# Performance work log

Hardware: AMD Instinct MI355X
Metric: run time of the kernel (lower is better)

## Reference

```python
import jax, jax.numpy as jnp
import numpy as np

DF, DK, DG, NR = 1024, 64, 64, 16
DV = DF // NR  # 64
N = 1024       # num_rois


def setup_inputs() -> dict:
    key = jax.random.key(0)
    ks = jax.random.split(key, 12)
    def xavier(k, out_d, in_d):
        lim = float(np.sqrt(6.0 / (in_d + out_d)))
        return jax.random.uniform(k, (out_d, in_d), jnp.float32, -lim, lim)
    return {
        "x": jax.random.normal(ks[0], (N, DF), jnp.float32),
        "position_embedding": jax.random.uniform(ks[1], (N, N, DG), jnp.float32),
        "Wq": xavier(ks[2], DK * NR, DF), "bq": jnp.zeros((DK * NR,), jnp.float32),
        "Wk": xavier(ks[3], DK * NR, DF), "bk": jnp.zeros((DK * NR,), jnp.float32),
        "Wv": xavier(ks[4], DF, DF),     "bv": jnp.zeros((DF,), jnp.float32),
        "Wg": xavier(ks[5], NR, DG),     "bg": jnp.zeros((NR,), jnp.float32),
        "Wy": xavier(ks[6], DF, DF),     "by": jnp.zeros((DF,), jnp.float32),
    }


def reference(x, position_embedding, Wq, bq, Wk, bk, Wv, bv, Wg, bg, Wy, by):
    n = x.shape[0]
    # geometry bias: linear -> relu -> clamp_min(1e-6) -> log, then head-major
    g = jnp.einsum('ijd,hd->hij', position_embedding, Wg) + bg[:, None, None]  # [Nr, N, N]
    g = jnp.log(jnp.maximum(jax.nn.relu(g), 1e-6))
    # projections, reshaped to [Nr, N, d]
    Q = (x @ Wq.T + bq).reshape(n, NR, DK).transpose(1, 0, 2)   # [Nr, N, dk]
    K = (x @ Wk.T + bk).reshape(n, NR, DK).transpose(1, 0, 2)   # [Nr, N, dk]
    V = (x @ Wv.T + bv).reshape(n, NR, DV).transpose(1, 0, 2)   # [Nr, N, dv]
    scores = jnp.einsum('hnd,hmd->hnm', Q, K) + g               # no 1/sqrt(dk) scaling (faithful)
    attn = jax.nn.softmax(scores, axis=2)
    Y = jnp.einsum('hnm,hmd->hnd', attn, V)                      # [Nr, N, dv]
    Y = Y.transpose(1, 0, 2).reshape(n, DF)
    y = Y @ Wy.T + by
    return x + y
```

## Files before the change

### kernel.cpp

```cpp
#include <hip/hip_runtime.h>
#include <hip/hip_bf16.h>


typedef __bf16 bf16_t;
typedef _Float16 f16_t;
typedef __attribute__((ext_vector_type(8))) __bf16 bf16x8;
typedef __attribute__((ext_vector_type(8))) _Float16 f16x8;
typedef __attribute__((ext_vector_type(4))) float f32x4;

__device__ inline bf16_t f2b(float f) {
    unsigned u = __builtin_bit_cast(unsigned, f);
    unsigned r = u + 0x7fffu + ((u >> 16) & 1u);
    unsigned short h = (unsigned short)(r >> 16);
    return __builtin_bit_cast(bf16_t, h);
}

__global__ __launch_bounds__(256) void fused_g_proj_k(
        const float* __restrict__ pe, const float* __restrict__ Wg, const float* __restrict__ bg,
        f16_t* __restrict__ Wout,
        const float* __restrict__ x,
        const float* __restrict__ Wq, const float* __restrict__ bq, bf16_t* __restrict__ Qb,
        const float* __restrict__ Wk, const float* __restrict__ bk, bf16_t* __restrict__ Kb,
        const float* __restrict__ Wv, const float* __restrict__ bv, bf16_t* __restrict__ Vb) {
    __shared__ char smem_raw[20480];
    const int bid = blockIdx.x;
    const int t = threadIdx.x;

    if (bid < 768) {
        bf16_t (*As)[64][40] = (bf16_t(*)[64][40])smem_raw;
        bf16_t (*Bs)[64][40] = (bf16_t(*)[64][40])(smem_raw + 10240);
        const int z = bid >> 8, rem = bid & 255;
        const float* B = (z == 0) ? Wq : (z == 1) ? Wk : Wv;
        const float* bias = (z == 0) ? bq : (z == 1) ? bk : bv;
        bf16_t* outp = (z == 0) ? Qb : (z == 1) ? Kb : Vb;
        const int m0 = (rem >> 4) * 64, n0 = (rem & 15) * 64;
        const int lr = t >> 2, lq = t & 3;

        auto stage = [&](bf16_t (*dst)[64][40], const float* __restrict__ Sp, int row0, int buf, int k0) {
            const float* p = Sp + (long)(row0 + lr) * 1024 + k0 + lq * 8;
            float4 u0 = *(const float4*)p;
            float4 u1 = *(const float4*)(p + 4);
            bf16x8 v;
            v[0] = f2b(u0.x); v[1] = f2b(u0.y); v[2] = f2b(u0.z); v[3] = f2b(u0.w);
            v[4] = f2b(u1.x); v[5] = f2b(u1.y); v[6] = f2b(u1.z); v[7] = f2b(u1.w);
            *(bf16x8*)&dst[buf][lr][lq * 8] = v;
        };

        const int wid = t >> 6, lane = t & 63;
        const int wm = (wid >> 1) * 32, wn = (wid & 1) * 32;
        const int ml = lane & 15, kl = (lane >> 4) * 8;
        f32x4 acc[2][2] = {};

        stage(As, x, m0, 0, 0);
        stage(Bs, B, n0, 0, 0);
        __syncthreads();
        for (int kt = 0; kt < 32; kt++) {
            const int buf = kt & 1;
            if (kt + 1 < 32) { stage(As, x, m0, buf ^ 1, (kt + 1) * 32); stage(Bs, B, n0, buf ^ 1, (kt + 1) * 32); }
            bf16x8 a0 = *(const bf16x8*)&As[buf][wm + ml][kl];
            bf16x8 a1 = *(const bf16x8*)&As[buf][wm + 16 + ml][kl];
            bf16x8 b0 = *(const bf16x8*)&Bs[buf][wn + ml][kl];
            bf16x8 b1 = *(const bf16x8*)&Bs[buf][wn + 16 + ml][kl];
            acc[0][0] = __builtin_amdgcn_mfma_f32_16x16x32_bf16(a0, b0, acc[0][0], 0, 0, 0);
            acc[0][1] = __builtin_amdgcn_mfma_f32_16x16x32_bf16(a0, b1, acc[0][1], 0, 0, 0);
            acc[1][0] = __builtin_amdgcn_mfma_f32_16x16x32_bf16(a1, b0, acc[1][0], 0, 0, 0);
            acc[1][1] = __builtin_amdgcn_mfma_f32_16x16x32_bf16(a1, b1, acc[1][1], 0, 0, 0);
            __syncthreads();
        }

#pragma unroll
        for (int mt = 0; mt < 2; mt++)
#pragma unroll
            for (int nt = 0; nt < 2; nt++) {
                f32x4 v = acc[mt][nt];
                const int rbase = m0 + wm + mt * 16 + ((lane >> 4) << 2);
                const int col = n0 + wn + nt * 16 + (lane & 15);
#pragma unroll
                for (int r = 0; r < 4; r++) {
                    const int row = rbase + r;
                    float val = v[r] + bias[col];
                    int h = col >> 6, d = col & 63;
                    if (z < 2) outp[((long)h << 16) + ((long)row << 6) + d] = f2b(val);
                    else       outp[((long)h << 16) + ((long)d << 10) + row] = f2b(val);
                }
            }
    } else {
        float4 (*tile4)[16] = (float4(*)[16])smem_raw;
        const long rowbase = (long)(bid - 768) * 64;
        const float4* src = (const float4*)(pe + rowbase * 64);
#pragma unroll
        for (int p = 0; p < 4; p++) {
            float4 v = src[p * 256 + t];
            int fi = p * 256 + t;
            int r = fi >> 4, c = fi & 15;
            tile4[r][c ^ (r & 15)] = v;
        }
        __syncthreads();
        const int r = t & 63;
        const int hbu = __builtin_amdgcn_readfirstlane((t >> 6) << 2);
        const float* wg0 = Wg + hbu * 64;
        const float* wg1 = wg0 + 64;
        const float* wg2 = wg0 + 128;
        const float* wg3 = wg0 + 192;
        float a0 = bg[hbu + 0], a1 = bg[hbu + 1], a2 = bg[hbu + 2], a3 = bg[hbu + 3];
#pragma unroll
        for (int dq = 0; dq < 16; dq++) {
            float4 pv = tile4[r][dq ^ (r & 15)];
            float4 w0 = *(const float4*)(wg0 + dq * 4);
            float4 w1 = *(const float4*)(wg1 + dq * 4);
            float4 w2 = *(const float4*)(wg2 + dq * 4);
            float4 w3 = *(const float4*)(wg3 + dq * 4);
            a0 += pv.x * w0.x + pv.y * w0.y + pv.z * w0.z + pv.w * w0.w;
            a1 += pv.x * w1.x + pv.y * w1.y + pv.z * w1.z + pv.w * w1.w;
            a2 += pv.x * w2.x + pv.y * w2.y + pv.z * w2.z + pv.w * w2.w;
            a3 += pv.x * w3.x + pv.y * w3.y + pv.z * w3.z + pv.w * w3.w;
        }
        Wout[(long)(hbu + 0) * 1048576 + rowbase + r] = (f16_t)fmaxf(a0, 1e-6f);
        Wout[(long)(hbu + 1) * 1048576 + rowbase + r] = (f16_t)fmaxf(a1, 1e-6f);
        Wout[(long)(hbu + 2) * 1048576 + rowbase + r] = (f16_t)fmaxf(a2, 1e-6f);
        Wout[(long)(hbu + 3) * 1048576 + rowbase + r] = (f16_t)fmaxf(a3, 1e-6f);
    }
}

__global__ __launch_bounds__(256) void gemmY_k(const bf16_t* __restrict__ A,
                                               const float* __restrict__ Bw,
                                               const float* __restrict__ bias,
                                               float* __restrict__ outp,
                                               const float* __restrict__ extra) {
    __shared__ bf16_t As[2][64][40];
    __shared__ bf16_t Bs[2][64][40];
    const int t = threadIdx.x;
    const int m0 = blockIdx.y * 64, n0 = blockIdx.x * 64;
    const int lr = t >> 2, lq = t & 3;

    auto stageA = [&](int buf, int k0) {
        const bf16_t* p = A + (long)(m0 + lr) * 1024 + k0 + lq * 8;
        *(bf16x8*)&As[buf][lr][lq * 8] = *(const bf16x8*)p;
    };
    auto stageB = [&](int buf, int k0) {
        const float* p = Bw + (long)(n0 + lr) * 1024 + k0 + lq * 8;
        float4 u0 = *(const float4*)p;
        float4 u1 = *(const float4*)(p + 4);
        bf16x8 v;
        v[0] = f2b(u0.x); v[1] = f2b(u0.y); v[2] = f2b(u0.z); v[3] = f2b(u0.w);
        v[4] = f2b(u1.x); v[5] = f2b(u1.y); v[6] = f2b(u1.z); v[7] = f2b(u1.w);
        *(bf16x8*)&Bs[buf][lr][lq * 8] = v;
    };

    const int wid = t >> 6, lane = t & 63;
    const int wm = (wid >> 1) * 32, wn = (wid & 1) * 32;
    const int ml = lane & 15, kl = (lane >> 4) * 8;
    f32x4 acc[2][2] = {};

    stageA(0, 0);
    stageB(0, 0);
    __syncthreads();
    for (int kt = 0; kt < 32; kt++) {
        const int buf = kt & 1;
        if (kt + 1 < 32) { stageA(buf ^ 1, (kt + 1) * 32); stageB(buf ^ 1, (kt + 1) * 32); }
        bf16x8 a0 = *(const bf16x8*)&As[buf][wm + ml][kl];
        bf16x8 a1 = *(const bf16x8*)&As[buf][wm + 16 + ml][kl];
        bf16x8 b0 = *(const bf16x8*)&Bs[buf][wn + ml][kl];
        bf16x8 b1 = *(const bf16x8*)&Bs[buf][wn + 16 + ml][kl];
        acc[0][0] = __builtin_amdgcn_mfma_f32_16x16x32_bf16(a0, b0, acc[0][0], 0, 0, 0);
        acc[0][1] = __builtin_amdgcn_mfma_f32_16x16x32_bf16(a0, b1, acc[0][1], 0, 0, 0);
        acc[1][0] = __builtin_amdgcn_mfma_f32_16x16x32_bf16(a1, b0, acc[1][0], 0, 0, 0);
        acc[1][1] = __builtin_amdgcn_mfma_f32_16x16x32_bf16(a1, b1, acc[1][1], 0, 0, 0);
        __syncthreads();
    }

#pragma unroll
    for (int mt = 0; mt < 2; mt++)
#pragma unroll
        for (int nt = 0; nt < 2; nt++) {
            f32x4 v = acc[mt][nt];
            const int rbase = m0 + wm + mt * 16 + ((lane >> 4) << 2);
            const int col = n0 + wn + nt * 16 + (lane & 15);
#pragma unroll
            for (int r = 0; r < 4; r++) {
                const int row = rbase + r;
                long idx = ((long)row << 10) + col;
                outp[idx] = v[r] + bias[col] + extra[idx];
            }
        }
}

__global__ __launch_bounds__(256) void attn_kernel(const bf16_t* __restrict__ Q,
                                                   const bf16_t* __restrict__ K,
                                                   const bf16_t* __restrict__ Vt,
                                                   const f16_t* __restrict__ Wf,
                                                   bf16_t* __restrict__ Y) {
    __shared__ bf16_t Qs[64][72];
    __shared__ bf16_t Ks[2][64][72];
    __shared__ bf16_t Vts[2][64][72];
    __shared__ f16_t  Ws[2][64][72];
    __shared__ bf16_t Ps[4][16][72];

    const int qt = blockIdx.x, h = blockIdx.y;
    const int t = threadIdx.x;
    const int w = t >> 6, lane = t & 63;
    const int ml = lane & 15, kq = lane >> 4;
    const int q0 = qt << 6;
    const int sr = t >> 2, sc = (t & 3) << 4;

    const bf16_t* Kh = K + ((long)h << 16);
    const bf16_t* Vh = Vt + ((long)h << 16);
    const f16_t*  Wh = Wf + ((long)h << 20) + ((long)(q0 + sr) << 10);

    {
        const bf16_t* src = Q + ((long)h << 16) + ((long)(q0 + sr) << 6) + sc;
        *(bf16x8*)&Qs[sr][sc]     = *(const bf16x8*)src;
        *(bf16x8*)&Qs[sr][sc + 8] = *(const bf16x8*)(src + 8);
        const bf16_t* ks = Kh + ((long)sr << 6) + sc;
        *(bf16x8*)&Ks[0][sr][sc]     = *(const bf16x8*)ks;
        *(bf16x8*)&Ks[0][sr][sc + 8] = *(const bf16x8*)(ks + 8);
        const bf16_t* vs = Vh + ((long)sr << 10) + sc;
        *(bf16x8*)&Vts[0][sr][sc]     = *(const bf16x8*)vs;
        *(bf16x8*)&Vts[0][sr][sc + 8] = *(const bf16x8*)(vs + 8);
        const f16_t* gs = Wh + sc;
        *(f16x8*)&Ws[0][sr][sc]     = *(const f16x8*)gs;
        *(f16x8*)&Ws[0][sr][sc + 8] = *(const f16x8*)(gs + 8);
    }
    __syncthreads();

    const bf16x8 aq0 = *(const bf16x8*)&Qs[(w << 4) + ml][kq * 8];
    const bf16x8 aq1 = *(const bf16x8*)&Qs[(w << 4) + ml][32 + kq * 8];

    f32x4 O[4] = {};
    float lsum[4] = {0.f, 0.f, 0.f, 0.f};

    int buf = 0;
    for (int kt = 0; kt < 16; kt++) {
        bf16x8 rk0, rk1, rv0, rv1;
        f16x8 rw0, rw1;
        const bool pf = (kt < 15);
        if (pf) {
            const int k0 = (kt + 1) << 6;
            const bf16_t* ks = Kh + ((long)(k0 + sr) << 6) + sc;
            rk0 = *(const bf16x8*)ks; rk1 = *(const bf16x8*)(ks + 8);
            const bf16_t* vs = Vh + ((long)sr << 10) + k0 + sc;
            rv0 = *(const bf16x8*)vs; rv1 = *(const bf16x8*)(vs + 8);
            const f16_t* gs = Wh + k0 + sc;
            rw0 = *(const f16x8*)gs; rw1 = *(const f16x8*)(gs + 8);
        }

        f32x4 s[4] = {};
#pragma unroll
        for (int c = 0; c < 4; c++) {
            bf16x8 bk0 = *(const bf16x8*)&Ks[buf][(c << 4) + ml][kq * 8];
            bf16x8 bk1 = *(const bf16x8*)&Ks[buf][(c << 4) + ml][32 + kq * 8];
            s[c] = __builtin_amdgcn_mfma_f32_16x16x32_bf16(aq0, bk0, s[c], 0, 0, 0);
            s[c] = __builtin_amdgcn_mfma_f32_16x16x32_bf16(aq1, bk1, s[c], 0, 0, 0);
        }
#pragma unroll
        for (int c = 0; c < 4; c++) {
#pragma unroll
            for (int r = 0; r < 4; r++) {
                float wv = (float)Ws[buf][(w << 4) + (kq << 2) + r][(c << 4) + ml];
                float p = __expf(s[c][r]) * wv;
                lsum[r] += p;
                Ps[w][(kq << 2) + r][(c << 4) + ml] = f2b(p);
            }
        }
        const bf16x8 pa0 = *(const bf16x8*)&Ps[w][ml][kq * 8];
        const bf16x8 pa1 = *(const bf16x8*)&Ps[w][ml][32 + kq * 8];
#pragma unroll
        for (int c = 0; c < 4; c++) {
            bf16x8 v0 = *(const bf16x8*)&Vts[buf][(c << 4) + ml][kq * 8];
            bf16x8 v1 = *(const bf16x8*)&Vts[buf][(c << 4) + ml][32 + kq * 8];
            O[c] = __builtin_amdgcn_mfma_f32_16x16x32_bf16(pa0, v0, O[c], 0, 0, 0);
            O[c] = __builtin_amdgcn_mfma_f32_16x16x32_bf16(pa1, v1, O[c], 0, 0, 0);
        }

        if (pf) {
            const int nb = buf ^ 1;
            *(bf16x8*)&Ks[nb][sr][sc]      = rk0;
            *(bf16x8*)&Ks[nb][sr][sc + 8]  = rk1;
            *(bf16x8*)&Vts[nb][sr][sc]     = rv0;
            *(bf16x8*)&Vts[nb][sr][sc + 8] = rv1;
            *(f16x8*)&Ws[nb][sr][sc]       = rw0;
            *(f16x8*)&Ws[nb][sr][sc + 8]   = rw1;
        }
        __syncthreads();
        buf ^= 1;
    }

#pragma unroll
    for (int r = 0; r < 4; r++) {
        float v = lsum[r];
        v += __shfl_xor(v, 1); v += __shfl_xor(v, 2);
        v += __shfl_xor(v, 4); v += __shfl_xor(v, 8);
        lsum[r] = 1.0f / v;
    }
    const int rowb = q0 + (w << 4) + (kq << 2);
    const int colb = (h << 6) + ml;
#pragma unroll
    for (int c = 0; c < 4; c++)
#pragma unroll
        for (int r = 0; r < 4; r++)
            Y[((long)(rowb + r) << 10) + colb + (c << 4)] = f2b(O[c][r] * lsum[r]);
}

extern "C" void kernel_launch(void* const* d_in, const int* in_sizes, int n_in,
                              void* d_out, int out_size, void* d_ws, size_t ws_size,
                              hipStream_t stream) {
    const float* x  = (const float*)d_in[0];
    const float* pe = (const float*)d_in[1];
    const float* Wq = (const float*)d_in[2];
    const float* bq = (const float*)d_in[3];
    const float* Wk = (const float*)d_in[4];
    const float* bk = (const float*)d_in[5];
    const float* Wv = (const float*)d_in[6];
    const float* bv = (const float*)d_in[7];
    const float* Wg = (const float*)d_in[8];
    const float* bg = (const float*)d_in[9];
    const float* Wy = (const float*)d_in[10];
    const float* by = (const float*)d_in[11];

    char* ws = (char*)d_ws;
    f16_t*  Wf = (f16_t*)ws;
    bf16_t* Qb = (bf16_t*)(ws + (32ul << 20));
    bf16_t* Kb = (bf16_t*)(ws + (34ul << 20));
    bf16_t* Vb = (bf16_t*)(ws + (36ul << 20));
    bf16_t* Yb = (bf16_t*)(ws + (38ul << 20));

    fused_g_proj_k<<<768 + 16384, 256, 0, stream>>>(pe, Wg, bg, Wf,
                                                    x, Wq, bq, Qb, Wk, bk, Kb, Wv, bv, Vb);
    attn_kernel<<<dim3(16, 16), 256, 0, stream>>>(Qb, Kb, Vb, Wf, Yb);
    gemmY_k<<<dim3(16, 16), 256, 0, stream>>>(Yb, Wy, by, (float*)d_out, x);
}
```

Measured before the change: 121.3 us.

## Process eight pe chunks per block with register prefetch of next chunk

The geometry-bias blocks each now loop over eight 64-row chunks of position_embedding instead of one, cutting that part of the grid from 16384 to 2048 blocks. Inside the loop, the next chunk's global loads are issued into registers before computing the current chunk, then written into LDS after a barrier. The intent is to cut block launch overhead and hide global load latency behind the FMA work. The cost is fewer resident blocks, more registers per thread and extra barriers. The kernel streams 256 MB of input, so it is probably bandwidth-bound and the gain may be small.

```diff
diff --git a/kernel.cpp b/kernel.cpp
--- a/kernel.cpp
+++ b/kernel.cpp
@@ -86,39 +86,64 @@
             }
     } else {
         float4 (*tile4)[16] = (float4(*)[16])smem_raw;
-        const long rowbase = (long)(bid - 768) * 64;
-        const float4* src = (const float4*)(pe + rowbase * 64);
-#pragma unroll
-        for (int p = 0; p < 4; p++) {
-            float4 v = src[p * 256 + t];
-            int fi = p * 256 + t;
-            int r = fi >> 4, c = fi & 15;
-            tile4[r][c ^ (r & 15)] = v;
-        }
-        __syncthreads();
+        const int gb = bid - 768;
+        const long chunk0 = (long)gb * 8;
         const int r = t & 63;
         const int hbu = __builtin_amdgcn_readfirstlane((t >> 6) << 2);
         const float* wg0 = Wg + hbu * 64;
         const float* wg1 = wg0 + 64;
         const float* wg2 = wg0 + 128;
         const float* wg3 = wg0 + 192;
-        float a0 = bg[hbu + 0], a1 = bg[hbu + 1], a2 = bg[hbu + 2], a3 = bg[hbu + 3];
-#pragma unroll
-        for (int dq = 0; dq < 16; dq++) {
-            float4 pv = tile4[r][dq ^ (r & 15)];
-            float4 w0 = *(const float4*)(wg0 + dq * 4);
-            float4 w1 = *(const float4*)(wg1 + dq * 4);
-            float4 w2 = *(const float4*)(wg2 + dq * 4);
-            float4 w3 = *(const float4*)(wg3 + dq * 4);
-            a0 += pv.x * w0.x + pv.y * w0.y + pv.z * w0.z + pv.w * w0.w;
-            a1 += pv.x * w1.x + pv.y * w1.y + pv.z * w1.z + pv.w * w1.w;
-            a2 += pv.x * w2.x + pv.y * w2.y + pv.z * w2.z + pv.w * w2.w;
-            a3 += pv.x * w3.x + pv.y * w3.y + pv.z * w3.z + pv.w * w3.w;
-        }
-        Wout[(long)(hbu + 0) * 1048576 + rowbase + r] = (f16_t)fmaxf(a0, 1e-6f);
-        Wout[(long)(hbu + 1) * 1048576 + rowbase + r] = (f16_t)fmaxf(a1, 1e-6f);
-        Wout[(long)(hbu + 2) * 1048576 + rowbase + r] = (f16_t)fmaxf(a2, 1e-6f);
-        Wout[(long)(hbu + 3) * 1048576 + rowbase + r] = (f16_t)fmaxf(a3, 1e-6f);
+        const float b0 = bg[hbu + 0], b1 = bg[hbu + 1], b2 = bg[hbu + 2], b3 = bg[hbu + 3];
+
+        {
+            const float4* src = (const float4*)(pe + chunk0 * 4096);
+#pragma unroll
+            for (int p = 0; p < 4; p++) {
+                float4 v = src[p * 256 + t];
+                int fi = p * 256 + t;
+                int rr = fi >> 4, c = fi & 15;
+                tile4[rr][c ^ (rr & 15)] = v;
+            }
+        }
+        __syncthreads();
+
+        for (int i = 0; i < 8; i++) {
+            float4 pf[4];
+            if (i < 7) {
+                const float4* src = (const float4*)(pe + (chunk0 + i + 1) * 4096);
+#pragma unroll
+                for (int p = 0; p < 4; p++) pf[p] = src[p * 256 + t];
+            }
+            float a0 = b0, a1 = b1, a2 = b2, a3 = b3;
+#pragma unroll
+            for (int dq = 0; dq < 16; dq++) {
+                float4 pv = tile4[r][dq ^ (r & 15)];
+                float4 w0 = *(const float4*)(wg0 + dq * 4);
+                float4 w1 = *(const float4*)(wg1 + dq * 4);
+                float4 w2 = *(const float4*)(wg2 + dq * 4);
+                float4 w3 = *(const float4*)(wg3 + dq * 4);
+                a0 += pv.x * w0.x + pv.y * w0.y + pv.z * w0.z + pv.w * w0.w;
+                a1 += pv.x * w1.x + pv.y * w1.y + pv.z * w1.z + pv.w * w1.w;
+                a2 += pv.x * w2.x + pv.y * w2.y + pv.z * w2.z + pv.w * w2.w;
+                a3 += pv.x * w3.x + pv.y * w3.y + pv.z * w3.z + pv.w * w3.w;
+            }
+            const long rowg = (chunk0 + i) * 64 + r;
+            Wout[(long)(hbu + 0) * 1048576 + rowg] = (f16_t)fmaxf(a0, 1e-6f);
+            Wout[(long)(hbu + 1) * 1048576 + rowg] = (f16_t)fmaxf(a1, 1e-6f);
+            Wout[(long)(hbu + 2) * 1048576 + rowg] = (f16_t)fmaxf(a2, 1e-6f);
+            Wout[(long)(hbu + 3) * 1048576 + rowg] = (f16_t)fmaxf(a3, 1e-6f);
+            __syncthreads();
+            if (i < 7) {
+#pragma unroll
+                for (int p = 0; p < 4; p++) {
+                    int fi = p * 256 + t;
+                    int rr = fi >> 4, c = fi & 15;
+                    tile4[rr][c ^ (rr & 15)] = pf[p];
+                }
+                __syncthreads();
+            }
+        }
     }
 }
 
@@ -324,8 +349,8 @@
     bf16_t* Vb = (bf16_t*)(ws + (36ul << 20));
     bf16_t* Yb = (bf16_t*)(ws + (38ul << 20));
 
-    fused_g_proj_k<<<768 + 16384, 256, 0, stream>>>(pe, Wg, bg, Wf,
-                                                    x, Wq, bq, Qb, Wk, bk, Kb, Wv, bv, Vb);
+    fused_g_proj_k<<<768 + 2048, 256, 0, stream>>>(pe, Wg, bg, Wf,
+                                                   x, Wq, bq, Qb, Wk, bk, Kb, Wv, bv, Vb);
     attn_kernel<<<dim3(16, 16), 256, 0, stream>>>(Qb, Kb, Vb, Wf, Yb);
     gemmY_k<<<dim3(16, 16), 256, 0, stream>>>(Yb, Wy, by, (float*)d_out, x);
 }
```

Measured after the change: 183.9 us. 51.6% more time.
